# Kernel tuning notes

Measured on AMD Instinct MI355X. Metric: run time of the kernel, lower is better.

## Reference

```python
import jax, jax.numpy as jnp
import numpy as np

B, S, D = 2, 2048, 1024
H = 16
HD = D // H  # 64


def setup_inputs() -> dict:
    key = jax.random.key(0)
    ks = jax.random.split(key, 5)
    scale = 1.0 / np.sqrt(D)
    return {
        "x": jax.random.normal(ks[0], (B, S, D), dtype=jnp.float32),
        "kqv_w": jax.random.normal(ks[1], (3 * D, D), dtype=jnp.float32) * scale,
        "kqv_b": jnp.zeros((3 * D,), dtype=jnp.float32),
        "out_w": jax.random.normal(ks[2], (D, D), dtype=jnp.float32) * scale,
        "out_b": jnp.zeros((D,), dtype=jnp.float32),
    }


def reference(x, kqv_w, kqv_b, out_w, out_b):
    # x: [B, S, D] -> torch code transposes to [S, B, D] (seq-first)
    xs = jnp.transpose(x, (1, 0, 2))  # [S, B, D]
    qkv = xs @ kqv_w.T + kqv_b        # [S, B, 3D]
    q, k, v = jnp.split(qkv, 3, axis=-1)  # each [S, B, D]

    def to_heads(t):
        # [S, B, D] -> [S, B*H, HD] -> [B*H, S, HD]
        return jnp.transpose(t.reshape(S, B * H, HD), (1, 0, 2))

    q, k, v = to_heads(q), to_heads(k), to_heads(v)
    # NOTE: original module computes self.scaling but never applies it -> no q scaling.
    attn = jnp.einsum('nqd,nkd->nqk', q, k)      # [B*H, S, S]
    attn = jax.nn.softmax(attn, axis=-1)
    out = jnp.einsum('nqk,nkd->nqd', attn, v)    # [B*H, S, HD]
    out = jnp.transpose(out, (1, 0, 2)).reshape(S, B, D)  # [S, B, D]
    out = out @ out_w.T + out_b
    return jnp.transpose(out, (1, 0, 2))  # [B, S, D]
```

## Files before the change

kernel.cpp:

```cpp
#include <hip/hip_runtime.h>

#define SEQ   2048
#define DIM   1024
#define NH    16
#define HD    64
#define BH    32
#define TOK   4096

typedef __bf16 bf16;
typedef __attribute__((ext_vector_type(4))) __bf16 bf16x4;
typedef __attribute__((ext_vector_type(8))) __bf16 bf16x8;
typedef __attribute__((ext_vector_type(4))) float f32x4;

#define LOG2E 1.44269504f

__device__ inline f32x4 mfma16(bf16x8 a, bf16x8 b, f32x4 c) {
  return __builtin_amdgcn_mfma_f32_16x16x32_bf16(a, b, c, 0, 0, 0);
}

__device__ inline void gload_lds16(const bf16* g, bf16* lds) {
  __builtin_amdgcn_global_load_lds(
      (const __attribute__((address_space(1))) void*)g,
      (__attribute__((address_space(3))) void*)lds, 16, 0, 0);
}

__device__ inline float exp2_hw(float x) {
  float r;
  asm("v_exp_f32 %0, %1" : "=v"(r) : "v"(x));
  return r;
}

__device__ inline void split8(const float* src, bf16x8& hi, bf16x8& lo) {
  float4 a = *(const float4*)src;
  float4 b = *(const float4*)(src + 4);
  float f[8] = {a.x, a.y, a.z, a.w, b.x, b.y, b.z, b.w};
#pragma unroll
  for (int i = 0; i < 8; ++i) {
    bf16 h = (bf16)f[i];
    hi[i] = h;
    lo[i] = (bf16)(f[i] - (float)h);
  }
}

__device__ inline void cast8(const float* src, bf16* dst) {
  float4 a = *(const float4*)src;
  float4 b = *(const float4*)(src + 4);
  bf16x8 v;
  v[0] = (bf16)a.x; v[1] = (bf16)a.y; v[2] = (bf16)a.z; v[3] = (bf16)a.w;
  v[4] = (bf16)b.x; v[5] = (bf16)b.y; v[6] = (bf16)b.z; v[7] = (bf16)b.w;
  *(bf16x8*)dst = v;
}

__global__ void prep_kernel(const float* __restrict__ x,
                            const float* __restrict__ kqv_w,
                            const float* __restrict__ out_w,
                            bf16* __restrict__ xh, bf16* __restrict__ xl,
                            bf16* __restrict__ wbf, bf16* __restrict__ wout) {
  const int NX8 = TOK * DIM / 8;
  const int NW8 = 3 * DIM * DIM / 8;
  const int NO8 = DIM * DIM / 8;
  int i = blockIdx.x * 256 + threadIdx.x;
  if (i < NX8) {
    bf16x8 h, l;
    split8(x + (size_t)i * 8, h, l);
    ((bf16x8*)xh)[i] = h;
    ((bf16x8*)xl)[i] = l;
  } else if (i < NX8 + NW8) {
    int j = i - NX8;
    cast8(kqv_w + (size_t)j * 8, wbf + (size_t)j * 8);
  } else if (i < NX8 + NW8 + NO8) {
    int j = i - NX8 - NW8;
    cast8(out_w + (size_t)j * 8, wout + (size_t)j * 8);
  }
}

__global__ __launch_bounds__(256) void gemm_qkv_ps(
    const bf16* __restrict__ xh, const bf16* __restrict__ xl,
    const bf16* __restrict__ wbf, const float* __restrict__ bias,
    bf16* __restrict__ qhh, bf16* __restrict__ qhl, bf16* __restrict__ kh,
    bf16* __restrict__ vT) {
  __shared__ bf16 AhA[64 * 64], AlA[64 * 64], BhA[64 * 64];
  __shared__ bf16 AhB[64 * 64], AlB[64 * 64], BhB[64 * 64];
  const int tid = threadIdx.x;
  const int lane = tid & 63;
  const int wave = tid >> 6;
  const int lr = lane & 15, lk = lane >> 4;
  const int bid = blockIdx.x;
  const int swz = (bid & 7) * 96 + (bid >> 3);
  const int m0 = (swz / 24) * 128, n0 = (swz % 24) * 128;
  const bool vpart = (n0 >= 2 * DIM);
  const int wm = (wave >> 1) * 64, wn = (wave & 1) * 64;
  f32x4 acc[4][4] = {};

  const int c0i = tid, c1i = 256 + tid;
  const int rp0 = c0i >> 3, lc0 = (c0i & 7) ^ (rp0 & 7);
  const int mm0 = (lc0 >> 2) * 64 + rp0, kk0 = (lc0 & 3) * 8;
  const int rp1 = c1i >> 3, lc1 = (c1i & 7) ^ (rp1 & 7);
  const int mm1 = (lc1 >> 2) * 64 + rp1, kk1 = (lc1 & 3) * 8;
  const bf16* pA0 = xh + (size_t)(m0 + mm0) * DIM + kk0;
  const bf16* pA1 = xh + (size_t)(m0 + mm1) * DIM + kk1;
  const bf16* pL0 = xl + (size_t)(m0 + mm0) * DIM + kk0;
  const bf16* pL1 = xl + (size_t)(m0 + mm1) * DIM + kk1;
  const bf16* pB0 = wbf + (size_t)(n0 + mm0) * DIM + kk0;
  const bf16* pB1 = wbf + (size_t)(n0 + mm1) * DIM + kk1;

  auto stageG = [&](bf16* Ah_, bf16* Al_, bf16* Bh_) {
    gload_lds16(pA0, Ah_ + c0i * 8);
    gload_lds16(pA1, Ah_ + c1i * 8);
    if (!vpart) {
      gload_lds16(pL0, Al_ + c0i * 8);
      gload_lds16(pL1, Al_ + c1i * 8);
    }
    gload_lds16(pB0, Bh_ + c0i * 8);
    gload_lds16(pB1, Bh_ + c1i * 8);
    pA0 += 32; pA1 += 32; pL0 += 32; pL1 += 32;
    pB0 += 32; pB1 += 32;
  };

  auto computeG = [&](const bf16* Ah, const bf16* Al, const bf16* Bh) {
    bf16x8 afh[4], afl[4], bfv[4];
#pragma unroll
    for (int i = 0; i < 4; ++i) {
      int m = wm + i * 16 + lr;
      int rp = m & 63;
      int pc = ((m >> 6) * 4 + lk) ^ (rp & 7);
      afh[i] = *(const bf16x8*)(Ah + rp * 64 + pc * 8);
    }
#pragma unroll
    for (int j = 0; j < 4; ++j) {
      int m = wn + j * 16 + lr;
      int rp = m & 63;
      int pc = ((m >> 6) * 4 + lk) ^ (rp & 7);
      bfv[j] = *(const bf16x8*)(Bh + rp * 64 + pc * 8);
    }
    __builtin_amdgcn_s_setprio(1);
#pragma unroll
    for (int i = 0; i < 4; ++i)
#pragma unroll
      for (int j = 0; j < 4; ++j)
        acc[i][j] = mfma16(afh[i], bfv[j], acc[i][j]);
    __builtin_amdgcn_s_setprio(0);
    if (!vpart) {
#pragma unroll
      for (int i = 0; i < 4; ++i) {
        int m = wm + i * 16 + lr;
        int rp = m & 63;
        int pc = ((m >> 6) * 4 + lk) ^ (rp & 7);
        afl[i] = *(const bf16x8*)(Al + rp * 64 + pc * 8);
      }
      __builtin_amdgcn_s_setprio(1);
#pragma unroll
      for (int i = 0; i < 4; ++i)
#pragma unroll
        for (int j = 0; j < 4; ++j)
          acc[i][j] = mfma16(afl[i], bfv[j], acc[i][j]);
      __builtin_amdgcn_s_setprio(0);
    }
  };

  stageG(AhA, AlA, BhA);
  __syncthreads();
  for (int k0 = 0; k0 < DIM; k0 += 64) {
    stageG(AhB, AlB, BhB);
    computeG(AhA, AlA, BhA);
    __syncthreads();
    if (k0 + 64 < DIM) {
      stageG(AhA, AlA, BhA);
    }
    computeG(AhB, AlB, BhB);
    __syncthreads();
  }

#pragma unroll
  for (int j = 0; j < 4; ++j) {
    int col = n0 + wn + j * 16 + lr;
    float bv = bias[col];
    int part = col >> 10, cc2 = col & 1023;
    int h = cc2 >> 6, d = cc2 & 63;
#pragma unroll
    for (int i = 0; i < 4; ++i) {
      int rowb = m0 + wm + i * 16 + lk * 4;
#pragma unroll
      for (int r = 0; r < 4; ++r) {
        int row = rowb + r;
        float val = acc[i][j][r] + bv;
        int b = row >> 11, s = row & 2047;
        int n = b * NH + h;
        size_t idx = ((size_t)n * SEQ + s) * HD + d;
        if (part == 0) {
          float vq = val * LOG2E;
          bf16 qh_ = (bf16)vq;
          qhh[idx] = qh_;
          qhl[idx] = (bf16)(vq - (float)qh_);
        } else if (part == 1) {
          kh[idx] = (bf16)val;
        } else {
          vT[((size_t)n * HD + d) * SEQ + s] = (bf16)val;
        }
      }
    }
  }
}

__global__ __launch_bounds__(256) void gemm_out(
    const bf16* __restrict__ A, const bf16* __restrict__ Bw,
    const float* __restrict__ bias, float* __restrict__ outF) {
  __shared__ bf16 AsA[64 * 64], BsA[64 * 64];
  __shared__ bf16 AsB[64 * 64], BsB[64 * 64];
  const int tid = threadIdx.x;
  const int lane = tid & 63;
  const int wave = tid >> 6;
  const int lr = lane & 15, lk = lane >> 4;
  const int m0 = blockIdx.y * 128, n0 = blockIdx.x * 128;
  const int wm = (wave >> 1) * 64, wn = (wave & 1) * 64;
  f32x4 acc[4][4] = {};

  const int c0i = tid, c1i = 256 + tid;
  const int rp0 = c0i >> 3, lc0 = (c0i & 7) ^ (rp0 & 7);
  const int mm0 = (lc0 >> 2) * 64 + rp0, kk0 = (lc0 & 3) * 8;
  const int rp1 = c1i >> 3, lc1 = (c1i & 7) ^ (rp1 & 7);
  const int mm1 = (lc1 >> 2) * 64 + rp1, kk1 = (lc1 & 3) * 8;
  const bf16* pA0 = A + (size_t)(m0 + mm0) * DIM + kk0;
  const bf16* pA1 = A + (size_t)(m0 + mm1) * DIM + kk1;
  const bf16* pB0 = Bw + (size_t)(n0 + mm0) * DIM + kk0;
  const bf16* pB1 = Bw + (size_t)(n0 + mm1) * DIM + kk1;

#define STAGEO(As_, Bs_)              \
  do {                                \
    gload_lds16(pA0, As_ + c0i * 8);  \
    gload_lds16(pA1, As_ + c1i * 8);  \
    gload_lds16(pB0, Bs_ + c0i * 8);  \
    gload_lds16(pB1, Bs_ + c1i * 8);  \
    pA0 += 32; pA1 += 32;             \
    pB0 += 32; pB1 += 32;             \
  } while (0)

  auto computeO = [&](const bf16* As, const bf16* Bs) {
    bf16x8 af[4], bfv[4];
#pragma unroll
    for (int i = 0; i < 4; ++i) {
      int m = wm + i * 16 + lr;
      int rp = m & 63;
      int pc = ((m >> 6) * 4 + lk) ^ (rp & 7);
      af[i] = *(const bf16x8*)(As + rp * 64 + pc * 8);
    }
#pragma unroll
    for (int j = 0; j < 4; ++j) {
      int m = wn + j * 16 + lr;
      int rp = m & 63;
      int pc = ((m >> 6) * 4 + lk) ^ (rp & 7);
      bfv[j] = *(const bf16x8*)(Bs + rp * 64 + pc * 8);
    }
    __builtin_amdgcn_s_setprio(1);
#pragma unroll
    for (int i = 0; i < 4; ++i)
#pragma unroll
      for (int j = 0; j < 4; ++j)
        acc[i][j] = mfma16(af[i], bfv[j], acc[i][j]);
    __builtin_amdgcn_s_setprio(0);
  };

  STAGEO(AsA, BsA);
  __syncthreads();
  for (int k0 = 0; k0 < DIM; k0 += 64) {
    STAGEO(AsB, BsB);
    computeO(AsA, BsA);
    __syncthreads();
    if (k0 + 64 < DIM) {
      STAGEO(AsA, BsA);
    }
    computeO(AsB, BsB);
    __syncthreads();
  }
#undef STAGEO

#pragma unroll
  for (int j = 0; j < 4; ++j) {
    int col = n0 + wn + j * 16 + lr;
    float bv = bias[col];
#pragma unroll
    for (int i = 0; i < 4; ++i) {
      int rowb = m0 + wm + i * 16 + lk * 4;
#pragma unroll
      for (int r = 0; r < 4; ++r)
        outF[(size_t)(rowb + r) * DIM + col] = acc[i][j][r] + bv;
    }
  }
}

__global__ __launch_bounds__(256) void attn_kernel(
    const bf16* __restrict__ qhh, const bf16* __restrict__ qhl,
    const bf16* __restrict__ kh, const bf16* __restrict__ vT,
    bf16* __restrict__ aout) {
  __shared__ bf16 KsA[64 * 64], VsA[64 * 64];
  __shared__ bf16 KsB[64 * 64], VsB[64 * 64];
  const int tid = threadIdx.x;
  const int lane = tid & 63;
  const int w = tid >> 6;
  const int lr = lane & 15, lk = lane >> 4;
  const int bid = blockIdx.x;
  const int swz = (bid & 7) * 64 + (bid >> 3);
  const int n = swz >> 4;
  const int q0 = (swz & 15) * 128 + w * 32;

  const bf16* qbh = qhh + ((size_t)n * SEQ + q0) * HD;
  const bf16* qbl = qhl + ((size_t)n * SEQ + q0) * HD;
  bf16x8 aqh[2][2], aql[2][2];
#pragma unroll
  for (int g = 0; g < 2; ++g) {
    aqh[g][0] = *(const bf16x8*)(qbh + (g * 16 + lr) * HD + lk * 8);
    aqh[g][1] = *(const bf16x8*)(qbh + (g * 16 + lr) * HD + 32 + lk * 8);
    aql[g][0] = *(const bf16x8*)(qbl + (g * 16 + lr) * HD + lk * 8);
    aql[g][1] = *(const bf16x8*)(qbl + (g * 16 + lr) * HD + 32 + lk * 8);
  }

  const int c0i = tid, c1i = 256 + tid;
  const int r0 = c0i >> 3, lc0 = ((c0i & 7) ^ (r0 & 7)) * 8;
  const int r1 = c1i >> 3, lc1 = ((c1i & 7) ^ (r1 & 7)) * 8;
  const size_t kbase = (size_t)n * SEQ * HD;
  const size_t vbase = (size_t)n * HD * SEQ;
  const bf16* pK0 = kh + kbase + (size_t)r0 * HD + lc0;
  const bf16* pK1 = kh + kbase + (size_t)r1 * HD + lc1;
  const bf16* pV0 = vT + vbase + (size_t)r0 * SEQ + lc0;
  const bf16* pV1 = vT + vbase + (size_t)r1 * SEQ + lc1;

  bf16x8 ones;
#pragma unroll
  for (int i = 0; i < 8; ++i) ones[i] = (bf16)1.0f;

  f32x4 o[2][4] = {};
  float lrow[2][4] = {};
  float mq[2] = {-1e30f, -1e30f};

#define STAGE(Ks_, Vs_)                   \
  do {                                    \
    gload_lds16(pK0, Ks_ + c0i * 8);      \
    gload_lds16(pK1, Ks_ + c1i * 8);      \
    gload_lds16(pV0, Vs_ + c0i * 8);      \
    gload_lds16(pV1, Vs_ + c1i * 8);      \
    pK0 += 64 * HD; pK1 += 64 * HD;       \
    pV0 += 64; pV1 += 64;                 \
  } while (0)

  auto compute = [&](const bf16* Ks, const bf16* Vs) {
    f32x4 sa[2][4] = {};
    __builtin_amdgcn_s_setprio(1);
#pragma unroll
    for (int j = 0; j < 4; ++j) {
      int row = j * 16 + lr;
      int c0 = (lk ^ (row & 7)) * 8;
      int c1 = ((4 + lk) ^ (row & 7)) * 8;
      const bf16* kr = Ks + row * 64;
      bf16x8 b0 = *(const bf16x8*)(kr + c0);
      bf16x8 b1 = *(const bf16x8*)(kr + c1);
#pragma unroll
      for (int g = 0; g < 2; ++g) {
        sa[g][j] = mfma16(b0, aqh[g][0], sa[g][j]);
        sa[g][j] = mfma16(b1, aqh[g][1], sa[g][j]);
        sa[g][j] = mfma16(b0, aql[g][0], sa[g][j]);
        sa[g][j] = mfma16(b1, aql[g][1], sa[g][j]);
      }
    }
    __builtin_amdgcn_s_setprio(0);

    float tmax[2];
#pragma unroll
    for (int g = 0; g < 2; ++g) {
      float t0 = fmaxf(fmaxf(sa[g][0][0], sa[g][0][1]), sa[g][0][2]);
      float t1 = fmaxf(fmaxf(sa[g][0][3], sa[g][1][0]), sa[g][1][1]);
      float t2 = fmaxf(fmaxf(sa[g][1][2], sa[g][1][3]), sa[g][2][0]);
      float t3 = fmaxf(fmaxf(sa[g][2][1], sa[g][2][2]), sa[g][2][3]);
      float t4 = fmaxf(fmaxf(sa[g][3][0], sa[g][3][1]), sa[g][3][2]);
      float tm = fmaxf(fmaxf(t0, t1), fmaxf(fmaxf(t2, t3), fmaxf(t4, sa[g][3][3])));
      tm = fmaxf(tm, __shfl_xor(tm, 16));
      tm = fmaxf(tm, __shfl_xor(tm, 32));
      tmax[g] = tm;
    }

    int flag = (tmax[0] > mq[0] + 11.5f) | (tmax[1] > mq[1] + 11.5f);
    if (__any(flag)) {
#pragma unroll
      for (int g = 0; g < 2; ++g) {
        float mnew = fmaxf(mq[g], tmax[g]);
        float sc = exp2_hw(mq[g] - mnew);
        mq[g] = mnew;
#pragma unroll
        for (int r = 0; r < 4; ++r) {
          float so = __shfl(sc, lk * 4 + r);
          lrow[g][r] *= so;
#pragma unroll
          for (int dj = 0; dj < 4; ++dj) o[g][dj][r] *= so;
        }
      }
    }

    bf16x8 pa[2][2];
#pragma unroll
    for (int g = 0; g < 2; ++g)
#pragma unroll
      for (int jj = 0; jj < 2; ++jj)
#pragma unroll
        for (int r = 0; r < 4; ++r) {
          pa[g][0][jj * 4 + r] = (bf16)exp2_hw(sa[g][jj][r] - mq[g]);
          pa[g][1][jj * 4 + r] = (bf16)exp2_hw(sa[g][2 + jj][r] - mq[g]);
        }

    __builtin_amdgcn_s_setprio(1);
    f32x4 ls[2] = {};
#pragma unroll
    for (int g = 0; g < 2; ++g) {
      ls[g] = mfma16(pa[g][0], ones, ls[g]);
      ls[g] = mfma16(pa[g][1], ones, ls[g]);
    }
#pragma unroll
    for (int dj = 0; dj < 4; ++dj) {
      int row = dj * 16 + lr;
      int rs = row & 7;
      const bf16* vr = Vs + row * 64;
      int h8 = (lk & 1) * 4;
      bf16x4 v00 = *(const bf16x4*)(vr + (((lk >> 1) + 0) ^ rs) * 8 + h8);
      bf16x4 v01 = *(const bf16x4*)(vr + (((lk >> 1) + 2) ^ rs) * 8 + h8);
      bf16x4 v10 = *(const bf16x4*)(vr + (((lk >> 1) + 4) ^ rs) * 8 + h8);
      bf16x4 v11 = *(const bf16x4*)(vr + (((lk >> 1) + 6) ^ rs) * 8 + h8);
      bf16x8 vf0, vf1;
#pragma unroll
      for (int i = 0; i < 4; ++i) {
        vf0[i] = v00[i]; vf0[4 + i] = v01[i];
        vf1[i] = v10[i]; vf1[4 + i] = v11[i];
      }
#pragma unroll
      for (int g = 0; g < 2; ++g) {
        o[g][dj] = mfma16(pa[g][0], vf0, o[g][dj]);
        o[g][dj] = mfma16(pa[g][1], vf1, o[g][dj]);
      }
    }
    __builtin_amdgcn_s_setprio(0);
#pragma unroll
    for (int g = 0; g < 2; ++g)
#pragma unroll
      for (int r = 0; r < 4; ++r) lrow[g][r] += ls[g][r];
  };

  STAGE(KsA, VsA);
  __syncthreads();

  for (int it = 0; it < SEQ / 64; it += 2) {
    STAGE(KsB, VsB);
    compute(KsA, VsA);
    __syncthreads();
    if (it + 2 < SEQ / 64) {
      STAGE(KsA, VsA);
    }
    compute(KsB, VsB);
    __syncthreads();
  }
#undef STAGE

  const int b = n >> 4, h = n & 15;
#pragma unroll
  for (int g = 0; g < 2; ++g)
#pragma unroll
    for (int r = 0; r < 4; ++r) {
      float inv = 1.0f / lrow[g][r];
      int s = q0 + g * 16 + lk * 4 + r;
      size_t base = ((size_t)(b * SEQ + s)) * DIM + h * HD;
#pragma unroll
      for (int j = 0; j < 4; ++j)
        aout[base + j * 16 + lr] = (bf16)(o[g][j][r] * inv);
    }
}

extern "C" void kernel_launch(void* const* d_in, const int* in_sizes, int n_in,
                              void* d_out, int out_size, void* d_ws, size_t ws_size,
                              hipStream_t stream) {
  const float* x     = (const float*)d_in[0];
  const float* kqv_w = (const float*)d_in[1];
  const float* kqv_b = (const float*)d_in[2];
  const float* out_w = (const float*)d_in[3];
  const float* out_b = (const float*)d_in[4];
  float* out = (float*)d_out;

  const size_t NX  = (size_t)TOK * DIM;
  const size_t NW  = (size_t)3 * DIM * DIM;
  const size_t NO  = (size_t)DIM * DIM;
  const size_t NKV = (size_t)BH * SEQ * HD;

  bf16* xh   = (bf16*)d_ws;
  bf16* xl   = xh + NX;
  bf16* wbf  = xl + NX;
  bf16* wout = wbf + NW;
  bf16* qhh  = wout + NO;
  bf16* qhl  = qhh + NKV;
  bf16* kh   = qhl + NKV;
  bf16* vT   = kh + NKV;
  bf16* aout = xh;

  const int PREP_BLOCKS = (int)((NX + NW + NO) / 8 / 256);
  prep_kernel<<<PREP_BLOCKS, 256, 0, stream>>>(x, kqv_w, out_w, xh, xl, wbf, wout);
  gemm_qkv_ps<<<768, 256, 0, stream>>>(xh, xl, wbf, kqv_b, qhh, qhl, kh, vT);
  attn_kernel<<<512, 256, 0, stream>>>(qhh, qhl, kh, vT, aout);
  gemm_out<<<dim3(DIM / 128, TOK / 128), 256, 0, stream>>>(aout, wout, out_b, out);
}
```

Before: 154.4 us.

## Stage V through registers with new LDS swizzle and remap out-GEMM block order

In the attention kernel, the V tile no longer goes straight to LDS via global_load_lds. It is loaded into registers, its 8-byte halves are swapped on odd lanes, and it is written to LDS after the compute of the current tile, with a new XOR read pattern meant to cut bank conflicts on the bf16x4 V fragment reads. The output GEMM moves to a 1D grid with a block-index swizzle to improve L2 reuse of tiles. In exchange, the register-staged path adds VGPR pressure and explicit LDS store instructions, and correctness depends on the write-side lane swap matching the new read offsets.

```diff
diff --git a/kernel.cpp b/kernel.cpp
--- a/kernel.cpp
+++ b/kernel.cpp
@@ -211,7 +211,9 @@
   const int lane = tid & 63;
   const int wave = tid >> 6;
   const int lr = lane & 15, lk = lane >> 4;
-  const int m0 = blockIdx.y * 128, n0 = blockIdx.x * 128;
+  const int bid = blockIdx.x;
+  const int swz = (bid & 7) * 32 + (bid >> 3);
+  const int m0 = (swz >> 3) * 128, n0 = (swz & 7) * 128;
   const int wm = (wave >> 1) * 64, wn = (wave & 1) * 64;
   f32x4 acc[4][4] = {};
 
@@ -323,6 +325,14 @@
   const bf16* pK1 = kh + kbase + (size_t)r1 * HD + lc1;
   const bf16* pV0 = vT + vbase + (size_t)r0 * SEQ + lc0;
   const bf16* pV1 = vT + vbase + (size_t)r1 * SEQ + lc1;
+  const bool vsw = (w & 1);
+
+  const int u0v = 2 * (lk >> 1) + (lk & 1);
+  const int xr = (2 * (lr & 7)) ^ (lr >> 3);
+  const int e0 = ((u0v) ^ xr) * 4;
+  const int e1 = ((u0v + 4) ^ xr) * 4;
+  const int e2 = ((u0v + 8) ^ xr) * 4;
+  const int e3 = ((u0v + 12) ^ xr) * 4;
 
   bf16x8 ones;
 #pragma unroll
@@ -332,14 +342,29 @@
   float lrow[2][4] = {};
   float mq[2] = {-1e30f, -1e30f};
 
-#define STAGE(Ks_, Vs_)                   \
+#define STAGE_K(Ks_)                      \
   do {                                    \
     gload_lds16(pK0, Ks_ + c0i * 8);      \
     gload_lds16(pK1, Ks_ + c1i * 8);      \
-    gload_lds16(pV0, Vs_ + c0i * 8);      \
-    gload_lds16(pV1, Vs_ + c1i * 8);      \
     pK0 += 64 * HD; pK1 += 64 * HD;       \
+  } while (0)
+
+#define VLOAD(a, b)                       \
+  do {                                    \
+    a = *(const uint4*)pV0;               \
+    b = *(const uint4*)pV1;               \
     pV0 += 64; pV1 += 64;                 \
+  } while (0)
+
+#define VWRITE(Vs_, a, b)                                      \
+  do {                                                         \
+    uint4 t0, t1;                                              \
+    if (vsw) {                                                 \
+      t0.x = a.z; t0.y = a.w; t0.z = a.x; t0.w = a.y;          \
+      t1.x = b.z; t1.y = b.w; t1.z = b.x; t1.w = b.y;          \
+    } else { t0 = a; t1 = b; }                                 \
+    *(uint4*)((char*)(Vs_) + c0i * 16) = t0;                   \
+    *(uint4*)((char*)(Vs_) + c1i * 16) = t1;                   \
   } while (0)
 
   auto compute = [&](const bf16* Ks, const bf16* Vs) {
@@ -415,13 +440,11 @@
 #pragma unroll
     for (int dj = 0; dj < 4; ++dj) {
       int row = dj * 16 + lr;
-      int rs = row & 7;
       const bf16* vr = Vs + row * 64;
-      int h8 = (lk & 1) * 4;
-      bf16x4 v00 = *(const bf16x4*)(vr + (((lk >> 1) + 0) ^ rs) * 8 + h8);
-      bf16x4 v01 = *(const bf16x4*)(vr + (((lk >> 1) + 2) ^ rs) * 8 + h8);
-      bf16x4 v10 = *(const bf16x4*)(vr + (((lk >> 1) + 4) ^ rs) * 8 + h8);
-      bf16x4 v11 = *(const bf16x4*)(vr + (((lk >> 1) + 6) ^ rs) * 8 + h8);
+      bf16x4 v00 = *(const bf16x4*)(vr + e0);
+      bf16x4 v01 = *(const bf16x4*)(vr + e1);
+      bf16x4 v10 = *(const bf16x4*)(vr + e2);
+      bf16x4 v11 = *(const bf16x4*)(vr + e3);
       bf16x8 vf0, vf1;
 #pragma unroll
       for (int i = 0; i < 4; ++i) {
@@ -441,20 +464,31 @@
       for (int r = 0; r < 4; ++r) lrow[g][r] += ls[g][r];
   };
 
-  STAGE(KsA, VsA);
+  uint4 va0, va1;
+  STAGE_K(KsA);
+  VLOAD(va0, va1);
+  VWRITE(VsA, va0, va1);
   __syncthreads();
 
   for (int it = 0; it < SEQ / 64; it += 2) {
-    STAGE(KsB, VsB);
+    STAGE_K(KsB);
+    uint4 vb0, vb1;
+    VLOAD(vb0, vb1);
     compute(KsA, VsA);
+    VWRITE(VsB, vb0, vb1);
     __syncthreads();
-    if (it + 2 < SEQ / 64) {
-      STAGE(KsA, VsA);
+    bool more = (it + 2 < SEQ / 64);
+    if (more) {
+      STAGE_K(KsA);
+      VLOAD(va0, va1);
     }
     compute(KsB, VsB);
+    if (more) VWRITE(VsA, va0, va1);
     __syncthreads();
   }
-#undef STAGE
+#undef STAGE_K
+#undef VLOAD
+#undef VWRITE
 
   const int b = n >> 4, h = n & 15;
 #pragma unroll
@@ -499,5 +533,5 @@
   prep_kernel<<<PREP_BLOCKS, 256, 0, stream>>>(x, kqv_w, out_w, xh, xl, wbf, wout);
   gemm_qkv_ps<<<768, 256, 0, stream>>>(xh, xl, wbf, kqv_b, qhh, qhl, kh, vT);
   attn_kernel<<<512, 256, 0, stream>>>(qhh, qhl, kh, vT, aout);
-  gemm_out<<<dim3(DIM / 128, TOK / 128), 256, 0, stream>>>(aout, wout, out_b, out);
-}
+  gemm_out<<<256, 256, 0, stream>>>(aout, wout, out_b, out);
+}
```

Measured after the change: 151.7 us. No clear change (-1.7%).
